# Kernel tuning notes

Hardware: AMD Instinct MI355X
Metric: run time of the kernel (lower is better)

The kernel has to match this reference:

```python
import jax, jax.numpy as jnp
import numpy as np

N_PATCH = 80
N_FFT = 160
PAD = N_FFT // 2 - N_PATCH // 2  # 40
D = 64       # n_delays
NC = 512     # candidate TFs
L = 0.0064   # physical patch size (m)
DX = 4e-05   # pixel size (m)
FWHM = 0.0015


def setup_inputs() -> dict:
    key = jax.random.key(0)
    k0, k1 = jax.random.split(key)
    patch_stack = jax.random.normal(k0, (1, D, N_PATCH, N_PATCH), jnp.float32)
    # Fourier coordinates (centered grid), as in get_fourier_coord(N=160, l=0.0064)
    f = np.fft.fftshift(np.fft.fftfreq(N_FFT, d=L / N_FFT)) * 2 * np.pi
    KX, KY = np.meshgrid(f, f, indexing='xy')
    k_rad = np.sqrt(KX ** 2 + KY ** 2)
    k2D = jnp.asarray(k_rad, jnp.float32)
    theta2D = jnp.asarray(np.arctan2(KY, KX), jnp.float32)
    # self.k: ifftshifted radial wavenumber, broadcast shape [1,1,160,160]
    k_loss = jnp.asarray(np.fft.ifftshift(k_rad), jnp.float32)[None, None]
    # Gaussian apodization window, sigma = fwhm/4e-5/sqrt(2 ln 2)
    sigma = FWHM / DX / np.sqrt(2.0 * np.log(2.0))
    c = np.arange(N_PATCH) - (N_PATCH - 1) / 2.0
    gx, gy = np.meshgrid(c, c)
    gaussian_window = jnp.asarray(
        np.exp(-(gx ** 2 + gy ** 2) / (2.0 * sigma ** 2)), jnp.float32)[None]
    delays = jnp.linspace(-5e-5, 5e-5, D).astype(jnp.float32)
    # candidate (dc, x, y) wavefront parameters
    cand_params = (jax.random.uniform(k1, (NC, 3), jnp.float32, -1.0, 1.0)
                   * jnp.array([1e-5, 5e-6, 5e-6], jnp.float32))
    return dict(patch_stack=patch_stack, gaussian_window=gaussian_window,
                delays=delays, k2D=k2D, theta2D=theta2D, k_loss=k_loss,
                cand_params=cand_params)


def reference(patch_stack, gaussian_window, delays, k2D, theta2D, k_loss, cand_params):
    n = patch_stack.shape[-1]
    pad = n // 2
    # window, zero-pad to double size, ifftshift, FFT2 -> Y [1, D, 2n, 2n]
    yw = patch_stack * gaussian_window
    ypad = jnp.pad(yw, ((0, 0), (0, 0), (pad, pad), (pad, pad)))
    Y = jnp.fft.fft2(jnp.fft.ifftshift(ypad, axes=(-2, -1)))
    Yabs_k = jnp.abs(Y) * k_loss

    def make_tf(p):
        dc, x, y = p[0], p[1], p[2]
        w = dc + x * jnp.cos(2.0 * theta2D) + y * jnp.sin(2.0 * theta2D)
        # (exp(-i k d) + exp(i k d)) / 2 == cos(k d)  (real-valued TF)
        phase = k2D[None] * (delays[:, None, None] - w[None])  # [D, 2n, 2n]
        return jnp.fft.ifftshift(jnp.cos(phase), axes=(-2, -1))[None]  # [1, D, 2n, 2n]

    def step(carry, p):
        best_loss, best_X, best_idx, idx = carry
        H = make_tf(p)
        rhs = jnp.sum(Y * H, axis=-3, keepdims=True)   # conj(H) == H (real)
        lhs = jnp.sum(H * H, axis=-3, keepdims=True)   # |H|^2
        X = rhs / lhs                                   # [1, 1, 2n, 2n] complex
        loss = jnp.mean((Yabs_k - jnp.abs(H * X) * k_loss) ** 2,
                        axis=(-3, -2, -1))[0]
        better = loss < best_loss
        carry = (jnp.where(better, loss, best_loss),
                 jnp.where(better, X, best_X),
                 jnp.where(better, idx, best_idx),
                 idx + 1)
        return carry, None

    init = (jnp.array(jnp.inf, jnp.float32),
            jnp.zeros((1, 1, 2 * n, 2 * n), jnp.complex64),
            jnp.array(0, jnp.int32), jnp.array(0, jnp.int32))
    (best_loss, best_X, best_idx, _), _ = jax.lax.scan(step, init, cand_params)

    img = jnp.fft.fftshift(jnp.fft.ifft2(best_X), axes=(-2, -1))
    best_x = jnp.real(img[..., pad:pad + n, pad:pad + n])  # crop_half
    best_params = cand_params[best_idx]
    return best_x, best_params, best_loss
```

## Files before the change

### kernel.cpp

```cpp
#include <hip/hip_runtime.h>

#define NF 160
#define NP 80
#define ND 64
#define NC 512
#define NV 81
#define NPIXH (NF*NV)
#define NPIXP 13056
#define NSTR 1632
#define STRIPE 8
#define RECQ 21
#define BT 128
#define CPT 4
#define TWO_PI 6.283185307179586f

#define IP_AR 0
#define IP_AI 1
#define IP_BR 2
#define IP_BI 3
#define IP_P  4
#define IP_Q  5
#define IP_R  6
#define IP_C2T 7
#define IP_S2T 8
#define IP_K  9
#define NPRM 10

__device__ __forceinline__ void rot(float& c, float& s, float stc, float sts) {
  float t1 = s * sts;
  float t2 = s * stc;
  float cn = fmaf(c, stc, -t1);
  s = fmaf(c, sts, t2);
  c = cn;
}

__device__ __forceinline__ void start_i_pow(int n, float& c, float& s) {
  switch (n & 3) {
    case 0: c = 1.f; s = 0.f; break;
    case 1: c = 0.f; s = 1.f; break;
    case 2: c = -1.f; s = 0.f; break;
    default: c = 0.f; s = -1.f; break;
  }
}

__global__ __launch_bounds__(256) void k_fft_x(const float* __restrict__ patch,
                                               const float* __restrict__ gw,
                                               float2* __restrict__ T) {
  int idx = blockIdx.x * 256 + threadIdx.x;
  int v = idx % NV;
  int a = (idx / NV) % NP;
  int d = idx / (NV * NP);
  float c, s;
  start_i_pow(v, c, s);
  float stc, sts;
  sincosf(-TWO_PI * (float)v / (float)NF, &sts, &stc);
  const float* prow = patch + (size_t)(d * NP + a) * NP;
  const float* grow = gw + a * NP;
  float accR = 0.f, accI = 0.f;
#pragma unroll 4
  for (int b = 0; b < NP; ++b) {
    float f = prow[b] * grow[b];
    accR = fmaf(f, c, accR);
    accI = fmaf(f, s, accI);
    rot(c, s, stc, sts);
  }
  T[idx] = make_float2(accR, accI);
}

__global__ __launch_bounds__(256) void k_fft_y(const float2* __restrict__ T,
                                               float2* __restrict__ Y) {
  int idx = blockIdx.x * 256 + threadIdx.x;
  int v = idx % NV;
  int ug = (idx / NV) % 40;
  int d = idx / (NV * 40);
  float c[4], s[4], aR[4], aI[4], stc[4], sts[4];
#pragma unroll
  for (int j = 0; j < 4; ++j) {
    int u = ug * 4 + j;
    start_i_pow(u, c[j], s[j]);
    sincosf(-TWO_PI * (float)u / (float)NF, &sts[j], &stc[j]);
    aR[j] = 0.f; aI[j] = 0.f;
  }
  const float2* Tb = T + (size_t)(d * NP) * NV + v;
#pragma unroll 4
  for (int a = 0; a < NP; ++a) {
    float2 t = Tb[(size_t)a * NV];
#pragma unroll
    for (int j = 0; j < 4; ++j) {
      aR[j] = fmaf(t.x, c[j], aR[j]);
      aR[j] = fmaf(-t.y, s[j], aR[j]);
      aI[j] = fmaf(t.x, s[j], aI[j]);
      aI[j] = fmaf(t.y, c[j], aI[j]);
      rot(c[j], s[j], stc[j], sts[j]);
    }
  }
#pragma unroll
  for (int j = 0; j < 4; ++j) {
    int u = ug * 4 + j;
    Y[((size_t)d * NF + u) * NV + v] = make_float2(aR[j], aI[j]);
  }
}

__global__ __launch_bounds__(256) void k_prep(const float2* __restrict__ Y,
                                              const float* __restrict__ delays,
                                              const float* __restrict__ kloss,
                                              const float* __restrict__ theta,
                                              float4* __restrict__ rec4,
                                              float* __restrict__ prm) {
  int p = blockIdx.x * 256 + threadIdx.x;
  if (p >= NPIXH) {
#pragma unroll
    for (int jj = 0; jj < 16; ++jj)
      rec4[(size_t)jj * NPIXP + p] = make_float4(0.f, 0.f, 0.f, 0.f);
    rec4[(size_t)16 * NPIXP + p] = make_float4(0.f, 0.f, 0.f, 0.f);
    rec4[(size_t)17 * NPIXP + p] = make_float4(1.f, 0.f, 1.f, 0.f);
    rec4[(size_t)18 * NPIXP + p] = make_float4(0.f, 0.f, 0.f, 0.f);
    rec4[(size_t)19 * NPIXP + p] = make_float4(1.f, 0.f, 1.f, 0.f);
    rec4[(size_t)20 * NPIXP + p] = make_float4(2.f, 0.f, 0.f, 0.f);
    prm[IP_AR * NPIXP + p] = 0.f;  prm[IP_AI * NPIXP + p] = 0.f;
    prm[IP_BR * NPIXP + p] = 0.f;  prm[IP_BI * NPIXP + p] = 0.f;
    prm[IP_P * NPIXP + p] = 1.f;   prm[IP_Q * NPIXP + p] = 0.f;
    prm[IP_R * NPIXP + p] = 1.f;   prm[IP_C2T * NPIXP + p] = 0.f;
    prm[IP_S2T * NPIXP + p] = 0.f; prm[IP_K * NPIXP + p] = 0.f;
    return;
  }
  int u = p / NV, v = p % NV;
  float k = kloss[u * NF + v];
  float th = theta[((u + 80) % NF) * NF + ((v + 80) % NF)];
  float c2t = cosf(2.f * th), s2t = sinf(2.f * th);
  float w;
  if (v == 0 || v == 80) {
    if (u == 0 || u == 80) w = 1.f;
    else if (u < 80) w = 2.f;
    else w = 0.f;
  } else w = 2.f;
  float d0 = delays[0], d1 = delays[1];
  float sd0f, cd0f;
  sincosf(k * d0, &sd0f, &cd0f);
  float stc, sts;
  sincosf(k * (d1 - d0), &sts, &stc);
  float tcd = 2.f * stc;
  float cd = cd0f, sd = sd0f;
  float cd1s = 0.f, sd1s = 0.f;
  float Ar = 0.f, Ai = 0.f, Br = 0.f, Bi = 0.f, Pm = 0.f, Qm = 0.f, Rm = 0.f, S0 = 0.f;
  float yktmp[ND];
#pragma unroll
  for (int d = 0; d < ND; ++d) {
    if (d == 1) { cd1s = cd; sd1s = sd; }
    float2 y = Y[((size_t)d * NF + u) * NV + v];
    Ar = fmaf(y.x, cd, Ar);  Ai = fmaf(y.y, cd, Ai);
    Br = fmaf(y.x, sd, Br);  Bi = fmaf(y.y, sd, Bi);
    Pm = fmaf(cd, cd, Pm);  Qm = fmaf(cd, sd, Qm);  Rm = fmaf(sd, sd, Rm);
    float yk = sqrtf(fmaf(y.x, y.x, y.y * y.y)) * k;
    yktmp[d] = yk;
    S0 = fmaf(yk, yk, S0);
    rot(cd, sd, stc, sts);
  }
#pragma unroll
  for (int jj = 0; jj < 16; ++jj)
    rec4[(size_t)jj * NPIXP + p] = make_float4(yktmp[2 * jj], yktmp[63 - 2 * jj],
                                               yktmp[2 * jj + 1], yktmp[62 - 2 * jj]);
  rec4[(size_t)16 * NPIXP + p] = make_float4(Ar, Ai, Br, Bi);
  rec4[(size_t)17 * NPIXP + p] = make_float4(Pm, Qm, Rm, S0);
  rec4[(size_t)18 * NPIXP + p] = make_float4(c2t, s2t, k, w);
  rec4[(size_t)19 * NPIXP + p] = make_float4(cd0f, sd0f, cd1s, sd1s);
  rec4[(size_t)20 * NPIXP + p] = make_float4(tcd, 0.f, 0.f, 0.f);
  prm[IP_AR * NPIXP + p] = Ar;   prm[IP_AI * NPIXP + p] = Ai;
  prm[IP_BR * NPIXP + p] = Br;   prm[IP_BI * NPIXP + p] = Bi;
  prm[IP_P * NPIXP + p] = Pm;    prm[IP_Q * NPIXP + p] = Qm;
  prm[IP_R * NPIXP + p] = Rm;    prm[IP_C2T * NPIXP + p] = c2t;
  prm[IP_S2T * NPIXP + p] = s2t; prm[IP_K * NPIXP + p] = k;
}

__global__ __launch_bounds__(BT) void k_cand(const float4* __restrict__ rec4,
                                             const float* __restrict__ cand,
                                             float* __restrict__ partial) {
  __shared__ float4 buf[STRIPE][RECQ];
  int t = threadIdx.x;
  int p0 = blockIdx.x * STRIPE;
  float dc[CPT], xx[CPT], yy[CPT], acc[CPT];
#pragma unroll
  for (int ci = 0; ci < CPT; ++ci) {
    int c = t + ci * BT;
    dc[ci] = cand[c * 3 + 0];
    xx[ci] = cand[c * 3 + 1];
    yy[ci] = cand[c * 3 + 2];
    acc[ci] = 0.f;
  }
  for (int q = t; q < STRIPE * RECQ; q += BT) {
    int px = q / RECQ, qq = q - px * RECQ;
    buf[px][qq] = rec4[(size_t)qq * NPIXP + (p0 + px)];
  }
  __syncthreads();
#pragma unroll
  for (int i = 0; i < STRIPE; ++i) {
    const float4* r = &buf[i][0];
    float4 pA = r[16];
    float4 pB = r[17];
    float4 pC = r[18];
    float4 pD = r[19];
    float tcd = r[20].x;
    float4 y0 = r[0];
    float A0[CPT], A1[CPT], B0[CPT], B1[CPT], M[CPT], F0[CPT], F1[CPT];
#pragma unroll
    for (int ci = 0; ci < CPT; ++ci) {
      float w_ = fmaf(xx[ci], pC.x, fmaf(yy[ci], pC.y, dc[ci]));
      float sw, cw;
      __sincosf(pC.z * w_, &sw, &cw);
      float rr = fmaf(cw, pA.x, sw * pA.z);
      float ri = fmaf(cw, pA.y, sw * pA.w);
      float lhs = fmaf(cw * cw, pB.x, fmaf(2.f * cw * sw, pB.y, sw * sw * pB.z));
      float rabs = __builtin_amdgcn_sqrtf(fmaf(rr, rr, ri * ri));
      float rl = __builtin_amdgcn_rcpf(lhs);
      float e = fmaf(-lhs, rl, 1.f);
      rl = fmaf(rl, e, rl);
      float kX = pC.z * rabs * rl;
      F0[ci] = fmaf(kX * kX, lhs, pB.w);
      F1[ci] = -2.f * kX;
      float t0 = pD.x * cw, u0 = pD.y * sw;
      float t1 = pD.z * cw, u1 = pD.w * sw;
      A0[ci] = t0 + u0;  B0[ci] = t0 - u0;
      A1[ci] = t1 + u1;  B1[ci] = t1 - u1;
      float m = y0.x * fabsf(A0[ci]);
      m = fmaf(y0.y, fabsf(B0[ci]), m);
      m = fmaf(y0.z, fabsf(A1[ci]), m);
      m = fmaf(y0.w, fabsf(B1[ci]), m);
      M[ci] = m;
    }
#pragma unroll
    for (int jj = 1; jj < 16; ++jj) {
      float4 yk = r[jj];
#pragma unroll
      for (int ci = 0; ci < CPT; ++ci) {
        float An = fmaf(tcd, A1[ci], -A0[ci]);
        float Bn = fmaf(tcd, B1[ci], -B0[ci]);
        float m = fmaf(yk.x, fabsf(An), M[ci]);
        m = fmaf(yk.y, fabsf(Bn), m);
        float An2 = fmaf(tcd, An, -A1[ci]);
        float Bn2 = fmaf(tcd, Bn, -B1[ci]);
        m = fmaf(yk.z, fabsf(An2), m);
        m = fmaf(yk.w, fabsf(Bn2), m);
        M[ci] = m;
        A0[ci] = An; A1[ci] = An2;
        B0[ci] = Bn; B1[ci] = Bn2;
      }
    }
#pragma unroll
    for (int ci = 0; ci < CPT; ++ci)
      acc[ci] = fmaf(fmaf(F1[ci], M[ci], F0[ci]), pC.w, acc[ci]);
  }
#pragma unroll
  for (int ci = 0; ci < CPT; ++ci)
    partial[(size_t)blockIdx.x * NC + t + ci * BT] = acc[ci];
}

__global__ __launch_bounds__(256) void k_sum(const float* __restrict__ partial,
                                             float* __restrict__ loss) {
  __shared__ float red[256];
  int c = blockIdx.x;
  float s = 0.f;
  for (int j = threadIdx.x; j < NSTR; j += 256)
    s += partial[(size_t)j * NC + c];
  red[threadIdx.x] = s;
  __syncthreads();
  for (int off = 128; off > 0; off >>= 1) {
    if (threadIdx.x < off) red[threadIdx.x] += red[threadIdx.x + off];
    __syncthreads();
  }
  if (threadIdx.x == 0) loss[c] = red[0];
}

__global__ __launch_bounds__(256) void k_amin_ifftu(const float* __restrict__ loss,
                                                    const float* __restrict__ prm,
                                                    const float* __restrict__ cand,
                                                    float* __restrict__ out,
                                                    float2* __restrict__ G) {
  __shared__ float sl[256];
  __shared__ int si[256];
  __shared__ float xr[NF], xi[NF];
  int c1 = threadIdx.x, c2 = threadIdx.x + 256;
  float s1 = loss[c1], s2 = loss[c2];
  float l; int i;
  if (s2 < s1) { l = s2; i = c2; } else { l = s1; i = c1; }
  sl[threadIdx.x] = l; si[threadIdx.x] = i;
  __syncthreads();
  for (int off = 128; off > 0; off >>= 1) {
    if (threadIdx.x < off) {
      float l2 = sl[threadIdx.x + off]; int i2 = si[threadIdx.x + off];
      if (l2 < sl[threadIdx.x] || (l2 == sl[threadIdx.x] && i2 < si[threadIdx.x])) {
        sl[threadIdx.x] = l2; si[threadIdx.x] = i2;
      }
    }
    __syncthreads();
  }
  int bi = si[0];
  if (blockIdx.x == 0 && threadIdx.x == 0) {
    out[6400] = cand[bi * 3 + 0];
    out[6401] = cand[bi * 3 + 1];
    out[6402] = cand[bi * 3 + 2];
    out[6403] = sl[0] * (1.f / 1638400.f);
  }
  int u = blockIdx.x;
  float dc = cand[bi * 3 + 0], xx = cand[bi * 3 + 1], yy = cand[bi * 3 + 2];
  int v = threadIdx.x;
  if (v < NF) {
    float sign = 1.f;
    int ph;
    if (v <= 80) {
      ph = u * NV + v;
    } else {
      int u2 = (NF - u) % NF;
      ph = u2 * NV + (NF - v);
      sign = -1.f;
    }
    float Ar = prm[IP_AR * NPIXP + ph], Ai = prm[IP_AI * NPIXP + ph];
    float Br = prm[IP_BR * NPIXP + ph], Bi = prm[IP_BI * NPIXP + ph];
    float Pm = prm[IP_P * NPIXP + ph], Qm = prm[IP_Q * NPIXP + ph], Rm = prm[IP_R * NPIXP + ph];
    float c2t = prm[IP_C2T * NPIXP + ph], s2t = prm[IP_S2T * NPIXP + ph];
    float k = prm[IP_K * NPIXP + ph];
    float w_ = fmaf(xx, c2t, fmaf(yy, s2t, dc));
    float sw, cw;
    sincosf(k * w_, &sw, &cw);
    float rr = fmaf(cw, Ar, sw * Br);
    float ri = fmaf(cw, Ai, sw * Bi);
    float lhs = fmaf(cw * cw, Pm, fmaf(2.f * cw * sw, Qm, sw * sw * Rm));
    xr[v] = rr / lhs;
    xi[v] = sign * ri / lhs;
  }
  __syncthreads();
  int b = threadIdx.x;
  if (b < NP) {
    int xb = (b + 120) % NF;
    float stc, sts;
    sincosf(TWO_PI * (float)xb / (float)NF, &sts, &stc);
    float c = 1.f, s = 0.f, accR = 0.f, accI = 0.f;
#pragma unroll 4
    for (int vv = 0; vv < NF; ++vv) {
      float xrv = xr[vv], xiv = xi[vv];
      accR = fmaf(xrv, c, accR); accR = fmaf(-xiv, s, accR);
      accI = fmaf(xrv, s, accI); accI = fmaf(xiv, c, accI);
      rot(c, s, stc, sts);
    }
    G[(size_t)u * NP + b] = make_float2(accR, accI);
  }
}

__global__ __launch_bounds__(64) void k_ifft_y(const float2* __restrict__ G,
                                               float* __restrict__ out) {
  int idx = blockIdx.x * 64 + threadIdx.x;
  int b = idx % NP;
  int a = idx / NP;
  int ya = (a + 120) % NF;
  float stc, sts;
  sincosf(TWO_PI * (float)ya / (float)NF, &sts, &stc);
  float c = 1.f, s = 0.f, accR = 0.f;
#pragma unroll 4
  for (int u = 0; u < NF; ++u) {
    float2 g = G[(size_t)u * NP + b];
    accR = fmaf(g.x, c, accR);
    accR = fmaf(-g.y, s, accR);
    rot(c, s, stc, sts);
  }
  out[idx] = accR * (1.f / 25600.f);
}

extern "C" void kernel_launch(void* const* d_in, const int* in_sizes, int n_in,
                              void* d_out, int out_size, void* d_ws, size_t ws_size,
                              hipStream_t stream) {
  (void)in_sizes; (void)n_in; (void)out_size; (void)ws_size;
  const float* patch  = (const float*)d_in[0];
  const float* gw     = (const float*)d_in[1];
  const float* delays = (const float*)d_in[2];
  const float* theta  = (const float*)d_in[4];
  const float* kloss  = (const float*)d_in[5];
  const float* cand   = (const float*)d_in[6];
  float* out = (float*)d_out;

  char* ws = (char*)d_ws;
  size_t off = 0;
  float2* Y = (float2*)(ws + off);      off += (size_t)ND * NF * NV * 8;
  float2* T = (float2*)(ws + off);      off += (size_t)ND * NP * NV * 8;
  float4* rec4 = (float4*)(ws + off);   off += (size_t)RECQ * NPIXP * 16;
  float* prm = (float*)(ws + off);      off += (size_t)NPRM * NPIXP * 4;
  float* partial = (float*)(ws + off);  off += (size_t)NSTR * NC * 4;
  float* loss = (float*)(ws + off);     off += (size_t)NC * 4;
  float2* G = (float2*)(ws + off);      off += (size_t)NF * NP * 8;

  hipLaunchKernelGGL(k_fft_x, dim3((ND * NP * NV) / 256), dim3(256), 0, stream, patch, gw, T);
  hipLaunchKernelGGL(k_fft_y, dim3((ND * 40 * NV) / 256), dim3(256), 0, stream, T, Y);
  hipLaunchKernelGGL(k_prep, dim3(NPIXP / 256), dim3(256), 0, stream, Y, delays, kloss, theta, rec4, prm);
  hipLaunchKernelGGL(k_cand, dim3(NSTR), dim3(BT), 0, stream, rec4, cand, partial);
  hipLaunchKernelGGL(k_sum, dim3(NC), dim3(256), 0, stream, partial, loss);
  hipLaunchKernelGGL(k_amin_ifftu, dim3(NF), dim3(256), 0, stream, loss, prm, cand, out, G);
  hipLaunchKernelGGL(k_ifft_y, dim3(100), dim3(64), 0, stream, G, out);
}
```

Before: 105.3 us.

## Split prep and final inverse-FFT loops across more threads, prefetch rec4 in candidate loop

```diff
diff --git a/kernel.cpp b/kernel.cpp
--- a/kernel.cpp
+++ b/kernel.cpp
@@ -107,69 +107,98 @@
                                               const float* __restrict__ theta,
                                               float4* __restrict__ rec4,
                                               float* __restrict__ prm) {
-  int p = blockIdx.x * 256 + threadIdx.x;
-  if (p >= NPIXH) {
-#pragma unroll
-    for (int jj = 0; jj < 16; ++jj)
-      rec4[(size_t)jj * NPIXP + p] = make_float4(0.f, 0.f, 0.f, 0.f);
-    rec4[(size_t)16 * NPIXP + p] = make_float4(0.f, 0.f, 0.f, 0.f);
-    rec4[(size_t)17 * NPIXP + p] = make_float4(1.f, 0.f, 1.f, 0.f);
-    rec4[(size_t)18 * NPIXP + p] = make_float4(0.f, 0.f, 0.f, 0.f);
-    rec4[(size_t)19 * NPIXP + p] = make_float4(1.f, 0.f, 1.f, 0.f);
-    rec4[(size_t)20 * NPIXP + p] = make_float4(2.f, 0.f, 0.f, 0.f);
-    prm[IP_AR * NPIXP + p] = 0.f;  prm[IP_AI * NPIXP + p] = 0.f;
-    prm[IP_BR * NPIXP + p] = 0.f;  prm[IP_BI * NPIXP + p] = 0.f;
-    prm[IP_P * NPIXP + p] = 1.f;   prm[IP_Q * NPIXP + p] = 0.f;
-    prm[IP_R * NPIXP + p] = 1.f;   prm[IP_C2T * NPIXP + p] = 0.f;
-    prm[IP_S2T * NPIXP + p] = 0.f; prm[IP_K * NPIXP + p] = 0.f;
-    return;
-  }
-  int u = p / NV, v = p % NV;
-  float k = kloss[u * NF + v];
-  float th = theta[((u + 80) % NF) * NF + ((v + 80) % NF)];
-  float c2t = cosf(2.f * th), s2t = sinf(2.f * th);
-  float w;
-  if (v == 0 || v == 80) {
-    if (u == 0 || u == 80) w = 1.f;
-    else if (u < 80) w = 2.f;
-    else w = 0.f;
-  } else w = 2.f;
-  float d0 = delays[0], d1 = delays[1];
-  float sd0f, cd0f;
-  sincosf(k * d0, &sd0f, &cd0f);
-  float stc, sts;
-  sincosf(k * (d1 - d0), &sts, &stc);
-  float tcd = 2.f * stc;
-  float cd = cd0f, sd = sd0f;
-  float cd1s = 0.f, sd1s = 0.f;
-  float Ar = 0.f, Ai = 0.f, Br = 0.f, Bi = 0.f, Pm = 0.f, Qm = 0.f, Rm = 0.f, S0 = 0.f;
-  float yktmp[ND];
-#pragma unroll
-  for (int d = 0; d < ND; ++d) {
-    if (d == 1) { cd1s = cd; sd1s = sd; }
-    float2 y = Y[((size_t)d * NF + u) * NV + v];
-    Ar = fmaf(y.x, cd, Ar);  Ai = fmaf(y.y, cd, Ai);
-    Br = fmaf(y.x, sd, Br);  Bi = fmaf(y.y, sd, Bi);
-    Pm = fmaf(cd, cd, Pm);  Qm = fmaf(cd, sd, Qm);  Rm = fmaf(sd, sd, Rm);
-    float yk = sqrtf(fmaf(y.x, y.x, y.y * y.y)) * k;
-    yktmp[d] = yk;
-    S0 = fmaf(yk, yk, S0);
-    rot(cd, sd, stc, sts);
-  }
-#pragma unroll
-  for (int jj = 0; jj < 16; ++jj)
-    rec4[(size_t)jj * NPIXP + p] = make_float4(yktmp[2 * jj], yktmp[63 - 2 * jj],
-                                               yktmp[2 * jj + 1], yktmp[62 - 2 * jj]);
-  rec4[(size_t)16 * NPIXP + p] = make_float4(Ar, Ai, Br, Bi);
-  rec4[(size_t)17 * NPIXP + p] = make_float4(Pm, Qm, Rm, S0);
-  rec4[(size_t)18 * NPIXP + p] = make_float4(c2t, s2t, k, w);
-  rec4[(size_t)19 * NPIXP + p] = make_float4(cd0f, sd0f, cd1s, sd1s);
-  rec4[(size_t)20 * NPIXP + p] = make_float4(tcd, 0.f, 0.f, 0.f);
-  prm[IP_AR * NPIXP + p] = Ar;   prm[IP_AI * NPIXP + p] = Ai;
-  prm[IP_BR * NPIXP + p] = Br;   prm[IP_BI * NPIXP + p] = Bi;
-  prm[IP_P * NPIXP + p] = Pm;    prm[IP_Q * NPIXP + p] = Qm;
-  prm[IP_R * NPIXP + p] = Rm;    prm[IP_C2T * NPIXP + p] = c2t;
-  prm[IP_S2T * NPIXP + p] = s2t; prm[IP_K * NPIXP + p] = k;
+  __shared__ float ykl[32][65];
+  __shared__ float mom[8][32][9];
+  int t = threadIdx.x;
+  int dg = t >> 5;
+  int pl = t & 31;
+  int p = blockIdx.x * 32 + pl;
+  bool valid = p < NPIXH;
+  float k = 0.f, c2t = 0.f, s2t = 0.f, wgt = 0.f;
+  int u = 0, v = 0;
+  if (valid) {
+    u = p / NV; v = p - u * NV;
+    k = kloss[u * NF + v];
+    float th = theta[((u + 80) % NF) * NF + ((v + 80) % NF)];
+    c2t = cosf(2.f * th); s2t = sinf(2.f * th);
+    if (v == 0 || v == 80) {
+      if (u == 0 || u == 80) wgt = 1.f;
+      else if (u < 80) wgt = 2.f;
+      else wgt = 0.f;
+    } else wgt = 2.f;
+  }
+  float mAr = 0.f, mAi = 0.f, mBr = 0.f, mBi = 0.f;
+  float mP = 0.f, mQ = 0.f, mR = 0.f, mS = 0.f;
+#pragma unroll
+  for (int j = 0; j < 8; ++j) {
+    int d = dg * 8 + j;
+    float sd, cd;
+    sincosf(k * delays[d], &sd, &cd);
+    float yx = 0.f, yy = 0.f;
+    if (valid) {
+      float2 y = Y[((size_t)d * NF + u) * NV + v];
+      yx = y.x; yy = y.y;
+    }
+    mAr = fmaf(yx, cd, mAr);  mAi = fmaf(yy, cd, mAi);
+    mBr = fmaf(yx, sd, mBr);  mBi = fmaf(yy, sd, mBi);
+    mP = fmaf(cd, cd, mP);  mQ = fmaf(cd, sd, mQ);  mR = fmaf(sd, sd, mR);
+    float yk = sqrtf(fmaf(yx, yx, yy * yy)) * k;
+    ykl[pl][d] = yk;
+    mS = fmaf(yk, yk, mS);
+  }
+  mom[dg][pl][0] = mAr; mom[dg][pl][1] = mAi;
+  mom[dg][pl][2] = mBr; mom[dg][pl][3] = mBi;
+  mom[dg][pl][4] = mP;  mom[dg][pl][5] = mQ;
+  mom[dg][pl][6] = mR;  mom[dg][pl][7] = mS;
+  __syncthreads();
+  {
+    int pl2 = t >> 3, val = t & 7;
+    float s = 0.f;
+#pragma unroll
+    for (int g2 = 0; g2 < 8; ++g2) s += mom[g2][pl2][val];
+    mom[0][pl2][val] = s;
+  }
+  __syncthreads();
+  {
+    int pl3 = t >> 3, q2 = t & 7;
+    int p3 = blockIdx.x * 32 + pl3;
+#pragma unroll
+    for (int h = 0; h < 2; ++h) {
+      int jj = q2 * 2 + h;
+      float4 q = make_float4(ykl[pl3][2 * jj], ykl[pl3][63 - 2 * jj],
+                             ykl[pl3][2 * jj + 1], ykl[pl3][62 - 2 * jj]);
+      rec4[(size_t)jj * NPIXP + p3] = q;
+    }
+  }
+  if (dg == 0) {
+    float Ar = mom[0][pl][0], Ai = mom[0][pl][1];
+    float Br = mom[0][pl][2], Bi = mom[0][pl][3];
+    float Pm = mom[0][pl][4], Qm = mom[0][pl][5];
+    float Rm = mom[0][pl][6], S0 = mom[0][pl][7];
+    if (valid) {
+      float d0 = delays[0], d1 = delays[1];
+      float sd0f, cd0f, sd1f, cd1f;
+      sincosf(k * d0, &sd0f, &cd0f);
+      sincosf(k * d1, &sd1f, &cd1f);
+      float tcd = 2.f * cosf(k * (d1 - d0));
+      rec4[(size_t)16 * NPIXP + p] = make_float4(Ar, Ai, Br, Bi);
+      rec4[(size_t)17 * NPIXP + p] = make_float4(Pm, Qm, Rm, S0);
+      rec4[(size_t)18 * NPIXP + p] = make_float4(c2t, s2t, k, wgt);
+      rec4[(size_t)19 * NPIXP + p] = make_float4(cd0f, sd0f, cd1f, sd1f);
+      rec4[(size_t)20 * NPIXP + p] = make_float4(tcd, 0.f, 0.f, 0.f);
+      prm[IP_AR * NPIXP + p] = Ar;   prm[IP_AI * NPIXP + p] = Ai;
+      prm[IP_BR * NPIXP + p] = Br;   prm[IP_BI * NPIXP + p] = Bi;
+      prm[IP_P * NPIXP + p] = Pm;    prm[IP_Q * NPIXP + p] = Qm;
+      prm[IP_R * NPIXP + p] = Rm;    prm[IP_C2T * NPIXP + p] = c2t;
+      prm[IP_S2T * NPIXP + p] = s2t; prm[IP_K * NPIXP + p] = k;
+    } else {
+      rec4[(size_t)16 * NPIXP + p] = make_float4(0.f, 0.f, 0.f, 0.f);
+      rec4[(size_t)17 * NPIXP + p] = make_float4(1.f, 0.f, 1.f, 0.f);
+      rec4[(size_t)18 * NPIXP + p] = make_float4(0.f, 0.f, 0.f, 0.f);
+      rec4[(size_t)19 * NPIXP + p] = make_float4(1.f, 0.f, 1.f, 0.f);
+      rec4[(size_t)20 * NPIXP + p] = make_float4(2.f, 0.f, 0.f, 0.f);
+    }
+  }
 }
 
 __global__ __launch_bounds__(BT) void k_cand(const float4* __restrict__ rec4,
@@ -227,9 +256,11 @@
       m = fmaf(y0.w, fabsf(B1[ci]), m);
       M[ci] = m;
     }
+    float4 ykn = r[1];
 #pragma unroll
     for (int jj = 1; jj < 16; ++jj) {
-      float4 yk = r[jj];
+      float4 yk = ykn;
+      if (jj < 15) ykn = r[jj + 1];
 #pragma unroll
       for (int ci = 0; ci < CPT; ++ci) {
         float An = fmaf(tcd, A1[ci], -A0[ci]);
@@ -345,23 +376,35 @@
   }
 }
 
-__global__ __launch_bounds__(64) void k_ifft_y(const float2* __restrict__ G,
-                                               float* __restrict__ out) {
-  int idx = blockIdx.x * 64 + threadIdx.x;
+__global__ __launch_bounds__(256) void k_ifft_y(const float2* __restrict__ G,
+                                                float* __restrict__ out) {
+  __shared__ float red[4][65];
+  int t = threadIdx.x;
+  int o = t & 63;
+  int slc = t >> 6;
+  int idx = blockIdx.x * 64 + o;
   int b = idx % NP;
   int a = idx / NP;
   int ya = (a + 120) % NF;
   float stc, sts;
   sincosf(TWO_PI * (float)ya / (float)NF, &sts, &stc);
-  float c = 1.f, s = 0.f, accR = 0.f;
+  float c, s;
+  start_i_pow(ya * slc, c, s);
+  float accR = 0.f;
+  const float2* Gb = G + (size_t)(slc * 40) * NP + b;
 #pragma unroll 4
-  for (int u = 0; u < NF; ++u) {
-    float2 g = G[(size_t)u * NP + b];
+  for (int j = 0; j < 40; ++j) {
+    float2 g = Gb[(size_t)j * NP];
     accR = fmaf(g.x, c, accR);
     accR = fmaf(-g.y, s, accR);
     rot(c, s, stc, sts);
   }
-  out[idx] = accR * (1.f / 25600.f);
+  red[slc][o] = accR;
+  __syncthreads();
+  if (t < 64) {
+    float s4 = ((red[0][t] + red[1][t]) + (red[2][t] + red[3][t]));
+    out[blockIdx.x * 64 + t] = s4 * (1.f / 25600.f);
+  }
 }
 
 extern "C" void kernel_launch(void* const* d_in, const int* in_sizes, int n_in,
@@ -388,9 +431,9 @@
 
   hipLaunchKernelGGL(k_fft_x, dim3((ND * NP * NV) / 256), dim3(256), 0, stream, patch, gw, T);
   hipLaunchKernelGGL(k_fft_y, dim3((ND * 40 * NV) / 256), dim3(256), 0, stream, T, Y);
-  hipLaunchKernelGGL(k_prep, dim3(NPIXP / 256), dim3(256), 0, stream, Y, delays, kloss, theta, rec4, prm);
+  hipLaunchKernelGGL(k_prep, dim3(408), dim3(256), 0, stream, Y, delays, kloss, theta, rec4, prm);
   hipLaunchKernelGGL(k_cand, dim3(NSTR), dim3(BT), 0, stream, rec4, cand, partial);
   hipLaunchKernelGGL(k_sum, dim3(NC), dim3(256), 0, stream, partial, loss);
   hipLaunchKernelGGL(k_amin_ifftu, dim3(NF), dim3(256), 0, stream, loss, prm, cand, out, G);
-  hipLaunchKernelGGL(k_ifft_y, dim3(100), dim3(64), 0, stream, G, out);
-}
+  hipLaunchKernelGGL(k_ifft_y, dim3(100), dim3(256), 0, stream, G, out);
+}
```

Result: faster. 94.72 us (-10.0%).
